# Performance work log

Hardware: AMD Instinct MI355X
Metric: run time of the kernel (lower is better)

## Reference

```python
import jax, jax.numpy as jnp
import numpy as np

S_LIST = (0.015, 0.02, 0.04, 0.08)
EPS = 1e-6
LOG_EPS = float(np.log(EPS))


def _ema_filtfilt(x, s):
    """scipy.signal.filtfilt([s], [1, s-1], x, axis=-1, padtype=None).

    Forward pass: y[n] = (1-s)*y[n-1] + s*x[n], with scipy's lfilter_zi*x[0]
    initial condition, which makes y[0] = x[0] exactly. Then the same filter
    is run backward (flip, filter, flip), again with y2[0] = (flipped y)[0].
    Implemented as a parallel linear-recurrence via associative_scan.
    """
    def one_pass(v):
        a = jnp.full_like(v, 1.0 - s).at[..., 0].set(0.0)
        b = (s * v).at[..., 0].set(v[..., 0])
        def comb(c1, c2):
            a1, b1 = c1
            a2, b2 = c2
            return a1 * a2, b1 * a2 + b2
        _, y = jax.lax.associative_scan(comb, (a, b), axis=-1)
        return y

    y = one_pass(x)                       # forward
    y = jnp.flip(one_pass(jnp.flip(y, axis=-1)), axis=-1)  # backward
    return y


def setup_inputs() -> dict:
    key = jax.random.key(0)
    ks = jax.random.split(key, 5)
    B, C, F, T = 16, 1, 256, 4096
    K = len(S_LIST)
    x = jax.random.uniform(ks[0], (B, C, F, T), dtype=jnp.float32)
    log_alpha = jnp.log(jax.random.normal(ks[1], (F,), dtype=jnp.float32) * 0.1 + 1.0)
    log_delta = jnp.log(jax.random.normal(ks[2], (F,), dtype=jnp.float32) * 0.1 + 1.0)
    log_r = jnp.log(jax.random.normal(ks[3], (F,), dtype=jnp.float32) * 0.1 + 1.0)
    z_ks = jax.random.normal(ks[4], (K, F), dtype=jnp.float32) * 0.1 + np.log(1.0 / K)
    return {"x": x, "log_alpha": log_alpha, "log_delta": log_delta,
            "log_r": log_r, "z_ks": z_ks}


def reference(x, log_alpha, log_delta, log_r, z_ks):
    # per-frequency params broadcast over [B, C, F, T]
    alpha = jnp.exp(log_alpha)[None, None, :, None]
    delta = jnp.exp(log_delta)[None, None, :, None]
    r = jnp.exp(log_r)[None, None, :, None]
    ez = jnp.exp(z_ks)
    w_ks = ez / jnp.sum(ez)  # [K, F], normalized over ALL entries (as in source)

    # multi-scale filtfilt smoothers; scipy path is detached from autodiff
    smoothers = jnp.stack([_ema_filtfilt(x, s) for s in S_LIST])  # [K,B,C,F,T]
    smoothers = jax.lax.stop_gradient(smoothers)

    M = jnp.einsum('kf,kbcft->bcft', w_ks, smoothers)
    M = jnp.exp(-alpha * (LOG_EPS + jnp.log1p(M / EPS)))
    return (x * M + delta) ** r - delta ** r
```

## Files before the change

kernel.cpp:

```cpp
#include <hip/hip_runtime.h>
#include <math.h>

#define T_DIM 4096
#define F_DIM 256
#define NROWS 4096
#define CHUNK 16
#define LOG2E 1.4426950408889634f

typedef float v2f __attribute__((ext_vector_type(2)));

__device__ __forceinline__ float fexp2(float v) { return __builtin_amdgcn_exp2f(v); }
__device__ __forceinline__ float flog2(float v) { return __builtin_amdgcn_logf(v); }
__device__ __forceinline__ float fexp(float v)  { return fexp2(v * LOG2E); }

__host__ __device__ constexpr float cpow(float b, int e) {
    float r = 1.0f;
    for (int i = 0; i < e; ++i) r *= b;
    return r;
}

template<int N> struct PT { float v[N]; };
template<int N>
__host__ __device__ constexpr PT<N> mk_pows(float a) {
    PT<N> t{}; float p = 1.0f;
    for (int i = 0; i < N; ++i) { t.v[i] = p; p *= a; }
    return t;
}

__device__ __forceinline__ v2f shfl_up2(v2f v, int d) {
    v2f r; r.x = __shfl_up(v.x, d, 64); r.y = __shfl_up(v.y, d, 64); return r;
}
__device__ __forceinline__ v2f shfl_down2(v2f v, int d) {
    v2f r; r.x = __shfl_down(v.x, d, 64); r.y = __shfl_down(v.y, d, 64); return r;
}

#define S0 0.015f
#define S1 0.02f
#define S2 0.04f
#define S3 0.08f

__global__ __launch_bounds__(256, 4)
void pcen_kernel(const float* __restrict__ x,
                 const float* __restrict__ log_alpha,
                 const float* __restrict__ log_delta,
                 const float* __restrict__ log_r,
                 const float* __restrict__ z_ks,
                 float* __restrict__ out)
{
#pragma clang fp contract(fast)
    const int tid  = threadIdx.x;
    const int lane = tid & 63;
    const int wid  = tid >> 6;
    const int rid  = blockIdx.x;
    const int f    = rid & (F_DIM - 1);

    __shared__ float sred[4];
    __shared__ v2f sEf0[4], sEf1[4];
    __shared__ v2f sEb0[4], sEb1[4];

    const size_t rbase = (size_t)rid * T_DIM;
    const size_t base  = rbase + (size_t)tid * CHUNK;
    const float4* xp = (const float4*)(x + base);
    float4 xq0 = xp[0], xq1 = xp[1], xq2 = xp[2], xq3 = xp[3];
    const float x0bc = x[rbase];
    const float v_la = log_alpha[f];
    const float v_ld = log_delta[f];
    const float v_lr = log_r[f];
    float zf[4];
    #pragma unroll
    for (int k = 0; k < 4; ++k) zf[k] = z_ks[k * F_DIM + f];

    float zs = fexp(z_ks[tid])       + fexp(z_ks[tid + 256])
             + fexp(z_ks[tid + 512]) + fexp(z_ks[tid + 768]);
    #pragma unroll
    for (int d = 32; d >= 1; d >>= 1) zs += __shfl_down(zs, d, 64);
    if (lane == 0) sred[wid] = zs;

    float xv[CHUNK];
    xv[0]=xq0.x; xv[1]=xq0.y; xv[2]=xq0.z; xv[3]=xq0.w;
    xv[4]=xq1.x; xv[5]=xq1.y; xv[6]=xq1.z; xv[7]=xq1.w;
    xv[8]=xq2.x; xv[9]=xq2.y; xv[10]=xq2.z; xv[11]=xq2.w;
    xv[12]=xq3.x; xv[13]=xq3.y; xv[14]=xq3.z; xv[15]=xq3.w;

    float ez[4];
    #pragma unroll
    for (int k = 0; k < 4; ++k) ez[k] = fexp(zf[k]);
    const float alpha = fexp(v_la);
    const float delta = fexp(v_ld);
    const float rr    = fexp(v_lr);
    const float dr    = fexp2(rr * flog2(delta));
    const float nalpha = -alpha;

    constexpr float a0 = 1.0f - S0, a1 = 1.0f - S1, a2 = 1.0f - S2, a3 = 1.0f - S3;
    constexpr float A0 = cpow(a0, CHUNK), A1 = cpow(a1, CHUNK);
    constexpr float A2 = cpow(a2, CHUNK), A3 = cpow(a3, CHUNK);
    constexpr float AW0 = cpow(a0, 64*CHUNK), AW1 = cpow(a1, 64*CHUNK);
    constexpr float AW2 = cpow(a2, 64*CHUNK), AW3 = cpow(a3, 64*CHUNK);
    constexpr PT<33> PA0 = mk_pows<33>(A0);
    constexpr PT<33> PA1 = mk_pows<33>(A1);
    constexpr PT<33> PA2 = mk_pows<33>(A2);
    constexpr PT<33> PA3 = mk_pows<33>(A3);
    constexpr float C1_0 = S0/(1.0f-a0*a0), C1_1 = S1/(1.0f-a1*a1);
    constexpr float C1_2 = S2/(1.0f-a2*a2), C1_3 = S3/(1.0f-a3*a3);
    constexpr float C2_0 = S0*S0/(1.0f-a0*a0), C2_1 = S1*S1/(1.0f-a1*a1);
    constexpr float C2_2 = S2*S2/(1.0f-a2*a2), C2_3 = S3*S3/(1.0f-a3*a3);

    const v2f av01 = {a0, a1}, av23 = {a2, a3};
    const v2f sv01 = {S0, S1}, sv23 = {S2, S3};
    const v2f AWv01 = {AW0, AW1}, AWv23 = {AW2, AW3};
    const float lgA0 = flog2(A0), lgA1 = flog2(A1), lgA2 = flog2(A2), lgA3 = flog2(A3);
    const v2f zero = {0.0f, 0.0f};

    v2f ef0, ef1, eb0, eb1;
    {
        v2f xa = {xv[0],  xv[0]};
        v2f xb = {xv[15], xv[15]};
        ef0 = sv01 * xa;  ef1 = sv23 * xa;
        eb0 = sv01 * xb;  eb1 = sv23 * xb;
        #pragma unroll
        for (int i = 1; i < CHUNK; ++i) {
            v2f xi = {xv[i],    xv[i]};
            v2f xj = {xv[15-i], xv[15-i]};
            ef0 = av01 * ef0 + sv01 * xi;
            ef1 = av23 * ef1 + sv23 * xi;
            eb0 = av01 * eb0 + sv01 * xj;
            eb1 = av23 * eb1 + sv23 * xj;
        }
    }

    #pragma unroll
    for (int st = 0; st < 6; ++st) {
        const int d = 1 << st;
        const v2f Ad01 = {PA0.v[d], PA1.v[d]};
        const v2f Ad23 = {PA2.v[d], PA3.v[d]};
        v2f tf0 = shfl_up2(ef0, d);
        v2f tf1 = shfl_up2(ef1, d);
        v2f tb0 = shfl_down2(eb0, d);
        v2f tb1 = shfl_down2(eb1, d);
        if (lane >= d)      { ef0 = Ad01 * tf0 + ef0; ef1 = Ad23 * tf1 + ef1; }
        if (lane < 64 - d)  { eb0 = Ad01 * tb0 + eb0; eb1 = Ad23 * tb1 + eb1; }
    }
    v2f exf0 = shfl_up2(ef0, 1),  exf1 = shfl_up2(ef1, 1);
    v2f exb0 = shfl_down2(eb0, 1), exb1 = shfl_down2(eb1, 1);

    if (lane == 63) { sEf0[wid] = ef0; sEf1[wid] = ef1; }
    if (lane == 0)  { sEb0[wid] = eb0; sEb1[wid] = eb1; }
    __syncthreads();

    const float invsum = 1.0f / (sred[0] + sred[1] + sred[2] + sred[3]);
    const float wk0 = ez[0]*invsum, wk1 = ez[1]*invsum, wk2 = ez[2]*invsum, wk3 = ez[3]*invsum;
    const v2f wf01 = {wk0*C1_0, wk1*C1_1};
    const v2f wf23 = {wk2*C1_2, wk3*C1_3};
    const float W2 = wk0*C2_0 + wk1*C2_1 + wk2*C2_2 + wk3*C2_3;

    const v2f x0v = {x0bc, x0bc};
    v2f Cf0 = x0v, Cf1 = x0v;
    for (int j = 0; j < wid; ++j) {
        Cf0 = AWv01 * Cf0 + sEf0[j];
        Cf1 = AWv23 * Cf1 + sEf1[j];
    }
    v2f yT0 = x0v, yT1 = x0v;
    #pragma unroll
    for (int j = 0; j < 4; ++j) {
        yT0 = AWv01 * yT0 + sEf0[j];
        yT1 = AWv23 * yT1 + sEf1[j];
    }
    v2f Cb0 = yT0, Cb1 = yT1;
    for (int j = 3; j > wid; --j) {
        Cb0 = AWv01 * Cb0 + sEb0[j];
        Cb1 = AWv23 * Cb1 + sEb1[j];
    }

    const float fl  = (float)lane;
    const float frl = (float)(63 - lane);
    v2f pAl01 = {fexp2(fl * lgA0),  fexp2(fl * lgA1)};
    v2f pAl23 = {fexp2(fl * lgA2),  fexp2(fl * lgA3)};
    v2f pAr01 = {fexp2(frl * lgA0), fexp2(frl * lgA1)};
    v2f pAr23 = {fexp2(frl * lgA2), fexp2(frl * lgA3)};
    v2f cpf0 = (lane == 0) ? zero : exf0;
    v2f cpf1 = (lane == 0) ? zero : exf1;
    v2f cnb0 = (lane == 63) ? zero : exb0;
    v2f cnb1 = (lane == 63) ? zero : exb1;
    v2f cf0 = cpf0 + pAl01 * Cf0;
    v2f cf1 = cpf1 + pAl23 * Cf1;
    v2f cb0 = cnb0 + pAr01 * Cb0;
    v2f cb1 = cnb1 + pAr23 * Cb1;

    float Macc[CHUNK];
    {
        v2f yf0 = cf0, yf1 = cf1;
        #pragma unroll
        for (int i = 0; i < CHUNK; ++i) {
            v2f xi = {xv[i], xv[i]};
            yf0 = av01 * yf0 + sv01 * xi;
            yf1 = av23 * yf1 + sv23 * xi;
            v2f mp = wf01 * yf0 + wf23 * yf1;
            Macc[i] = mp.x + mp.y;
        }
    }
    {
        v2f zb0 = cb0, zb1 = cb1;
        #pragma unroll
        for (int i = CHUNK-1; i >= 0; --i) {
            v2f xi = {xv[i], xv[i]};
            zb0 = av01 * zb0 + sv01 * xi;
            zb1 = av23 * zb1 + sv23 * xi;
            v2f mp = wf01 * zb0 + wf23 * zb1;
            Macc[i] = Macc[i] + (mp.x + mp.y) - W2 * xv[i];
        }
    }

    float4* op = (float4*)(out + base);
    #pragma unroll
    for (int j = 0; j < 4; ++j) {
        float o[4];
        #pragma unroll
        for (int q = 0; q < 4; ++q) {
            const int i = 4*j + q;
            const float Mp = fexp2(nalpha * flog2(Macc[i] + 1.0e-6f));
            const float v  = fmaf(xv[i], Mp, delta);
            o[q] = fexp2(rr * flog2(v)) - dr;
        }
        op[j] = make_float4(o[0], o[1], o[2], o[3]);
    }
}

extern "C" void kernel_launch(void* const* d_in, const int* in_sizes, int n_in,
                              void* d_out, int out_size, void* d_ws, size_t ws_size,
                              hipStream_t stream) {
    const float* x  = (const float*)d_in[0];
    const float* la = (const float*)d_in[1];
    const float* ld = (const float*)d_in[2];
    const float* lr = (const float*)d_in[3];
    const float* zk = (const float*)d_in[4];
    float* o = (float*)d_out;
    (void)in_sizes; (void)n_in; (void)out_size; (void)d_ws; (void)ws_size;
    hipLaunchKernelGGL(pcen_kernel, dim3(NROWS), dim3(256), 0, stream,
                       x, la, ld, lr, zk, o);
}
```

Measured before the change: 37.42 us.

## Process four rows per block with software-prefetched next-row loads

The kernel becomes persistent-style: each block handles four rows strided by 1024, which keeps the same frequency index f, and the grid shrinks to 1024 blocks. The next row's x data is loaded into registers while the current row is computed, so memory latency is hidden behind the scan math. Shared-memory carry buffers are double-buffered across rows. Per-row parameter setup and the z_ks softmax sum are now done once per block instead of once per row. The cost is higher register pressure from the prefetch registers and fewer blocks to spread across CUs.

```diff
diff --git a/kernel.cpp b/kernel.cpp
--- a/kernel.cpp
+++ b/kernel.cpp
@@ -4,6 +4,8 @@
 #define T_DIM 4096
 #define F_DIM 256
 #define NROWS 4096
+#define RPB 4
+#define RSTRIDE 1024
 #define CHUNK 16
 #define LOG2E 1.4426950408889634f
 
@@ -51,45 +53,11 @@
     const int tid  = threadIdx.x;
     const int lane = tid & 63;
     const int wid  = tid >> 6;
-    const int rid  = blockIdx.x;
-    const int f    = rid & (F_DIM - 1);
+    const int f    = blockIdx.x & (F_DIM - 1);
 
     __shared__ float sred[4];
-    __shared__ v2f sEf0[4], sEf1[4];
-    __shared__ v2f sEb0[4], sEb1[4];
-
-    const size_t rbase = (size_t)rid * T_DIM;
-    const size_t base  = rbase + (size_t)tid * CHUNK;
-    const float4* xp = (const float4*)(x + base);
-    float4 xq0 = xp[0], xq1 = xp[1], xq2 = xp[2], xq3 = xp[3];
-    const float x0bc = x[rbase];
-    const float v_la = log_alpha[f];
-    const float v_ld = log_delta[f];
-    const float v_lr = log_r[f];
-    float zf[4];
-    #pragma unroll
-    for (int k = 0; k < 4; ++k) zf[k] = z_ks[k * F_DIM + f];
-
-    float zs = fexp(z_ks[tid])       + fexp(z_ks[tid + 256])
-             + fexp(z_ks[tid + 512]) + fexp(z_ks[tid + 768]);
-    #pragma unroll
-    for (int d = 32; d >= 1; d >>= 1) zs += __shfl_down(zs, d, 64);
-    if (lane == 0) sred[wid] = zs;
-
-    float xv[CHUNK];
-    xv[0]=xq0.x; xv[1]=xq0.y; xv[2]=xq0.z; xv[3]=xq0.w;
-    xv[4]=xq1.x; xv[5]=xq1.y; xv[6]=xq1.z; xv[7]=xq1.w;
-    xv[8]=xq2.x; xv[9]=xq2.y; xv[10]=xq2.z; xv[11]=xq2.w;
-    xv[12]=xq3.x; xv[13]=xq3.y; xv[14]=xq3.z; xv[15]=xq3.w;
-
-    float ez[4];
-    #pragma unroll
-    for (int k = 0; k < 4; ++k) ez[k] = fexp(zf[k]);
-    const float alpha = fexp(v_la);
-    const float delta = fexp(v_ld);
-    const float rr    = fexp(v_lr);
-    const float dr    = fexp2(rr * flog2(delta));
-    const float nalpha = -alpha;
+    __shared__ v2f sEf0[2][4], sEf1[2][4];
+    __shared__ v2f sEb0[2][4], sEb1[2][4];
 
     constexpr float a0 = 1.0f - S0, a1 = 1.0f - S1, a2 = 1.0f - S2, a3 = 1.0f - S3;
     constexpr float A0 = cpow(a0, CHUNK), A1 = cpow(a1, CHUNK);
@@ -111,117 +79,174 @@
     const float lgA0 = flog2(A0), lgA1 = flog2(A1), lgA2 = flog2(A2), lgA3 = flog2(A3);
     const v2f zero = {0.0f, 0.0f};
 
-    v2f ef0, ef1, eb0, eb1;
+    const size_t tof = (size_t)tid * CHUNK;
+    float4 xq0, xq1, xq2, xq3; float x0bc;
     {
-        v2f xa = {xv[0],  xv[0]};
-        v2f xb = {xv[15], xv[15]};
-        ef0 = sv01 * xa;  ef1 = sv23 * xa;
-        eb0 = sv01 * xb;  eb1 = sv23 * xb;
-        #pragma unroll
-        for (int i = 1; i < CHUNK; ++i) {
-            v2f xi = {xv[i],    xv[i]};
-            v2f xj = {xv[15-i], xv[15-i]};
-            ef0 = av01 * ef0 + sv01 * xi;
-            ef1 = av23 * ef1 + sv23 * xi;
-            eb0 = av01 * eb0 + sv01 * xj;
-            eb1 = av23 * eb1 + sv23 * xj;
-        }
+        const float4* xp = (const float4*)(x + (size_t)blockIdx.x * T_DIM + tof);
+        xq0 = xp[0]; xq1 = xp[1]; xq2 = xp[2]; xq3 = xp[3];
+        x0bc = x[(size_t)blockIdx.x * T_DIM];
     }
 
+    const float v_la = log_alpha[f];
+    const float v_ld = log_delta[f];
+    const float v_lr = log_r[f];
+    float zf[4];
     #pragma unroll
-    for (int st = 0; st < 6; ++st) {
-        const int d = 1 << st;
-        const v2f Ad01 = {PA0.v[d], PA1.v[d]};
-        const v2f Ad23 = {PA2.v[d], PA3.v[d]};
-        v2f tf0 = shfl_up2(ef0, d);
-        v2f tf1 = shfl_up2(ef1, d);
-        v2f tb0 = shfl_down2(eb0, d);
-        v2f tb1 = shfl_down2(eb1, d);
-        if (lane >= d)      { ef0 = Ad01 * tf0 + ef0; ef1 = Ad23 * tf1 + ef1; }
-        if (lane < 64 - d)  { eb0 = Ad01 * tb0 + eb0; eb1 = Ad23 * tb1 + eb1; }
+    for (int k = 0; k < 4; ++k) zf[k] = z_ks[k * F_DIM + f];
+    {
+        float zs = fexp(z_ks[tid])       + fexp(z_ks[tid + 256])
+                 + fexp(z_ks[tid + 512]) + fexp(z_ks[tid + 768]);
+        #pragma unroll
+        for (int d = 32; d >= 1; d >>= 1) zs += __shfl_down(zs, d, 64);
+        if (lane == 0) sred[wid] = zs;
     }
-    v2f exf0 = shfl_up2(ef0, 1),  exf1 = shfl_up2(ef1, 1);
-    v2f exb0 = shfl_down2(eb0, 1), exb1 = shfl_down2(eb1, 1);
-
-    if (lane == 63) { sEf0[wid] = ef0; sEf1[wid] = ef1; }
-    if (lane == 0)  { sEb0[wid] = eb0; sEb1[wid] = eb1; }
-    __syncthreads();
-
-    const float invsum = 1.0f / (sred[0] + sred[1] + sred[2] + sred[3]);
-    const float wk0 = ez[0]*invsum, wk1 = ez[1]*invsum, wk2 = ez[2]*invsum, wk3 = ez[3]*invsum;
-    const v2f wf01 = {wk0*C1_0, wk1*C1_1};
-    const v2f wf23 = {wk2*C1_2, wk3*C1_3};
-    const float W2 = wk0*C2_0 + wk1*C2_1 + wk2*C2_2 + wk3*C2_3;
-
-    const v2f x0v = {x0bc, x0bc};
-    v2f Cf0 = x0v, Cf1 = x0v;
-    for (int j = 0; j < wid; ++j) {
-        Cf0 = AWv01 * Cf0 + sEf0[j];
-        Cf1 = AWv23 * Cf1 + sEf1[j];
-    }
-    v2f yT0 = x0v, yT1 = x0v;
+
+    v2f wf01, wf23;
+    float W2, nalpha, delta, rr, dr;
+
     #pragma unroll
-    for (int j = 0; j < 4; ++j) {
-        yT0 = AWv01 * yT0 + sEf0[j];
-        yT1 = AWv23 * yT1 + sEf1[j];
-    }
-    v2f Cb0 = yT0, Cb1 = yT1;
-    for (int j = 3; j > wid; --j) {
-        Cb0 = AWv01 * Cb0 + sEb0[j];
-        Cb1 = AWv23 * Cb1 + sEb1[j];
-    }
-
-    const float fl  = (float)lane;
-    const float frl = (float)(63 - lane);
-    v2f pAl01 = {fexp2(fl * lgA0),  fexp2(fl * lgA1)};
-    v2f pAl23 = {fexp2(fl * lgA2),  fexp2(fl * lgA3)};
-    v2f pAr01 = {fexp2(frl * lgA0), fexp2(frl * lgA1)};
-    v2f pAr23 = {fexp2(frl * lgA2), fexp2(frl * lgA3)};
-    v2f cpf0 = (lane == 0) ? zero : exf0;
-    v2f cpf1 = (lane == 0) ? zero : exf1;
-    v2f cnb0 = (lane == 63) ? zero : exb0;
-    v2f cnb1 = (lane == 63) ? zero : exb1;
-    v2f cf0 = cpf0 + pAl01 * Cf0;
-    v2f cf1 = cpf1 + pAl23 * Cf1;
-    v2f cb0 = cnb0 + pAr01 * Cb0;
-    v2f cb1 = cnb1 + pAr23 * Cb1;
-
-    float Macc[CHUNK];
-    {
-        v2f yf0 = cf0, yf1 = cf1;
-        #pragma unroll
-        for (int i = 0; i < CHUNK; ++i) {
-            v2f xi = {xv[i], xv[i]};
-            yf0 = av01 * yf0 + sv01 * xi;
-            yf1 = av23 * yf1 + sv23 * xi;
-            v2f mp = wf01 * yf0 + wf23 * yf1;
-            Macc[i] = mp.x + mp.y;
-        }
-    }
-    {
-        v2f zb0 = cb0, zb1 = cb1;
-        #pragma unroll
-        for (int i = CHUNK-1; i >= 0; --i) {
-            v2f xi = {xv[i], xv[i]};
-            zb0 = av01 * zb0 + sv01 * xi;
-            zb1 = av23 * zb1 + sv23 * xi;
-            v2f mp = wf01 * zb0 + wf23 * zb1;
-            Macc[i] = Macc[i] + (mp.x + mp.y) - W2 * xv[i];
-        }
-    }
-
-    float4* op = (float4*)(out + base);
-    #pragma unroll
-    for (int j = 0; j < 4; ++j) {
-        float o[4];
-        #pragma unroll
-        for (int q = 0; q < 4; ++q) {
-            const int i = 4*j + q;
-            const float Mp = fexp2(nalpha * flog2(Macc[i] + 1.0e-6f));
-            const float v  = fmaf(xv[i], Mp, delta);
-            o[q] = fexp2(rr * flog2(v)) - dr;
-        }
-        op[j] = make_float4(o[0], o[1], o[2], o[3]);
+    for (int r = 0; r < RPB; ++r) {
+        const size_t rid  = (size_t)blockIdx.x + (size_t)RSTRIDE * r;
+        const size_t base = rid * T_DIM + tof;
+
+        float4 nq0, nq1, nq2, nq3; float nx0;
+        if (r < RPB - 1) {
+            const float4* np = (const float4*)(x + (rid + RSTRIDE) * T_DIM + tof);
+            nq0 = np[0]; nq1 = np[1]; nq2 = np[2]; nq3 = np[3];
+            nx0 = x[(rid + RSTRIDE) * T_DIM];
+        }
+
+        float xv[CHUNK];
+        xv[0]=xq0.x; xv[1]=xq0.y; xv[2]=xq0.z; xv[3]=xq0.w;
+        xv[4]=xq1.x; xv[5]=xq1.y; xv[6]=xq1.z; xv[7]=xq1.w;
+        xv[8]=xq2.x; xv[9]=xq2.y; xv[10]=xq2.z; xv[11]=xq2.w;
+        xv[12]=xq3.x; xv[13]=xq3.y; xv[14]=xq3.z; xv[15]=xq3.w;
+
+        v2f ef0, ef1, eb0, eb1;
+        {
+            v2f xa = {xv[0],  xv[0]};
+            v2f xb = {xv[15], xv[15]};
+            ef0 = sv01 * xa;  ef1 = sv23 * xa;
+            eb0 = sv01 * xb;  eb1 = sv23 * xb;
+            #pragma unroll
+            for (int i = 1; i < CHUNK; ++i) {
+                v2f xi = {xv[i],    xv[i]};
+                v2f xj = {xv[15-i], xv[15-i]};
+                ef0 = av01 * ef0 + sv01 * xi;
+                ef1 = av23 * ef1 + sv23 * xi;
+                eb0 = av01 * eb0 + sv01 * xj;
+                eb1 = av23 * eb1 + sv23 * xj;
+            }
+        }
+
+        #pragma unroll
+        for (int st = 0; st < 6; ++st) {
+            const int d = 1 << st;
+            const v2f Ad01 = {PA0.v[d], PA1.v[d]};
+            const v2f Ad23 = {PA2.v[d], PA3.v[d]};
+            v2f tf0 = shfl_up2(ef0, d);
+            v2f tf1 = shfl_up2(ef1, d);
+            v2f tb0 = shfl_down2(eb0, d);
+            v2f tb1 = shfl_down2(eb1, d);
+            if (lane >= d)      { ef0 = Ad01 * tf0 + ef0; ef1 = Ad23 * tf1 + ef1; }
+            if (lane < 64 - d)  { eb0 = Ad01 * tb0 + eb0; eb1 = Ad23 * tb1 + eb1; }
+        }
+        v2f exf0 = shfl_up2(ef0, 1),  exf1 = shfl_up2(ef1, 1);
+        v2f exb0 = shfl_down2(eb0, 1), exb1 = shfl_down2(eb1, 1);
+
+        const int pb = r & 1;
+        if (lane == 63) { sEf0[pb][wid] = ef0; sEf1[pb][wid] = ef1; }
+        if (lane == 0)  { sEb0[pb][wid] = eb0; sEb1[pb][wid] = eb1; }
+        __syncthreads();
+
+        if (r == 0) {
+            const float invsum = 1.0f / (sred[0] + sred[1] + sred[2] + sred[3]);
+            const float wk0 = fexp(zf[0])*invsum, wk1 = fexp(zf[1])*invsum;
+            const float wk2 = fexp(zf[2])*invsum, wk3 = fexp(zf[3])*invsum;
+            wf01 = (v2f){wk0*C1_0, wk1*C1_1};
+            wf23 = (v2f){wk2*C1_2, wk3*C1_3};
+            W2 = wk0*C2_0 + wk1*C2_1 + wk2*C2_2 + wk3*C2_3;
+            const float alpha = fexp(v_la);
+            delta = fexp(v_ld);
+            rr    = fexp(v_lr);
+            dr    = fexp2(rr * flog2(delta));
+            nalpha = -alpha;
+        }
+
+        const v2f x0v = {x0bc, x0bc};
+        v2f Cf0 = x0v, Cf1 = x0v;
+        for (int j = 0; j < wid; ++j) {
+            Cf0 = AWv01 * Cf0 + sEf0[pb][j];
+            Cf1 = AWv23 * Cf1 + sEf1[pb][j];
+        }
+        v2f yT0 = x0v, yT1 = x0v;
+        #pragma unroll
+        for (int j = 0; j < 4; ++j) {
+            yT0 = AWv01 * yT0 + sEf0[pb][j];
+            yT1 = AWv23 * yT1 + sEf1[pb][j];
+        }
+        v2f Cb0 = yT0, Cb1 = yT1;
+        for (int j = 3; j > wid; --j) {
+            Cb0 = AWv01 * Cb0 + sEb0[pb][j];
+            Cb1 = AWv23 * Cb1 + sEb1[pb][j];
+        }
+
+        const float fl  = (float)lane;
+        const float frl = (float)(63 - lane);
+        v2f pAl01 = {fexp2(fl * lgA0),  fexp2(fl * lgA1)};
+        v2f pAl23 = {fexp2(fl * lgA2),  fexp2(fl * lgA3)};
+        v2f pAr01 = {fexp2(frl * lgA0), fexp2(frl * lgA1)};
+        v2f pAr23 = {fexp2(frl * lgA2), fexp2(frl * lgA3)};
+        v2f cpf0 = (lane == 0) ? zero : exf0;
+        v2f cpf1 = (lane == 0) ? zero : exf1;
+        v2f cnb0 = (lane == 63) ? zero : exb0;
+        v2f cnb1 = (lane == 63) ? zero : exb1;
+        v2f cf0 = cpf0 + pAl01 * Cf0;
+        v2f cf1 = cpf1 + pAl23 * Cf1;
+        v2f cb0 = cnb0 + pAr01 * Cb0;
+        v2f cb1 = cnb1 + pAr23 * Cb1;
+
+        float Macc[CHUNK];
+        {
+            v2f yf0 = cf0, yf1 = cf1;
+            #pragma unroll
+            for (int i = 0; i < CHUNK; ++i) {
+                v2f xi = {xv[i], xv[i]};
+                yf0 = av01 * yf0 + sv01 * xi;
+                yf1 = av23 * yf1 + sv23 * xi;
+                v2f mp = wf01 * yf0 + wf23 * yf1;
+                Macc[i] = mp.x + mp.y;
+            }
+        }
+        {
+            v2f zb0 = cb0, zb1 = cb1;
+            #pragma unroll
+            for (int i = CHUNK-1; i >= 0; --i) {
+                v2f xi = {xv[i], xv[i]};
+                zb0 = av01 * zb0 + sv01 * xi;
+                zb1 = av23 * zb1 + sv23 * xi;
+                v2f mp = wf01 * zb0 + wf23 * zb1;
+                Macc[i] = Macc[i] + (mp.x + mp.y) - W2 * xv[i];
+            }
+        }
+
+        float4* op = (float4*)(out + base);
+        #pragma unroll
+        for (int j = 0; j < 4; ++j) {
+            float o[4];
+            #pragma unroll
+            for (int q = 0; q < 4; ++q) {
+                const int i = 4*j + q;
+                const float Mp = fexp2(nalpha * flog2(Macc[i] + 1.0e-6f));
+                const float v  = fmaf(xv[i], Mp, delta);
+                o[q] = fexp2(rr * flog2(v)) - dr;
+            }
+            op[j] = make_float4(o[0], o[1], o[2], o[3]);
+        }
+
+        if (r < RPB - 1) {
+            xq0 = nq0; xq1 = nq1; xq2 = nq2; xq3 = nq3; x0bc = nx0;
+        }
     }
 }
 
@@ -235,6 +260,6 @@
     const float* zk = (const float*)d_in[4];
     float* o = (float*)d_out;
     (void)in_sizes; (void)n_in; (void)out_size; (void)d_ws; (void)ws_size;
-    hipLaunchKernelGGL(pcen_kernel, dim3(NROWS), dim3(256), 0, stream,
+    hipLaunchKernelGGL(pcen_kernel, dim3(NROWS / RPB), dim3(256), 0, stream,
                        x, la, ld, lr, zk, o);
 }
```

New measurement: 73.45 us. 96.3% more time.
